# Kernel optimization log

Measured on AMD Instinct MI355X. Metric: run time of the kernel, lower is better.

Reference implementation:

```python
import jax, jax.numpy as jnp
import numpy as np

BLOCK = 16
WINDOW = 6
NSEG = BLOCK - WINDOW + 1  # 11
ACT_TH = 0.1
IMP_TH = 0.1


def _gauss_kernel(size=7, sigma=7.0 / 6):
    m = (size - 1) / 2.0
    y, x = np.mgrid[-m:m + 1, -m:m + 1]
    h = np.exp(-(x * x + y * y) / (2.0 * sigma * sigma))
    h[h < np.finfo(h.dtype).eps * h.max()] = 0
    h /= h.sum()
    return jnp.asarray(h, dtype=jnp.float32)


def _normalize_with_gauss(img):
    # MSCN normalization: (img - mu) / (std + 1), gaussian 7x7 sigma=7/6, replicate pad
    k = _gauss_kernel()[None, None]  # [1,1,7,7]
    pad = 3
    p = jnp.pad(img, ((0, 0), (0, 0), (pad, pad), (pad, pad)), mode='edge')
    conv = lambda z: jax.lax.conv_general_dilated(z, k, (1, 1), 'VALID')
    mu = conv(p)
    mu2 = conv(p * p)
    std = jnp.sqrt(jnp.abs(mu2 - mu * mu))
    return (img - mu) / (std + 1.0)


def _seg_std_min(edge):
    # edge: [..., 16]; sliding windows of length 6 at offsets 0..10 (matches segment_edge)
    segs = jnp.stack([edge[..., i:i + WINDOW] for i in range(NSEG)], axis=-2)  # [...,11,6]
    return jnp.min(jnp.std(segs, axis=-1, ddof=1), axis=-1)


def _piqe_core(x):
    B, C, H, W = x.shape
    img = jnp.round(255.0 * x / jnp.max(x.reshape(B, -1), axis=-1)[:, None, None, None])
    col_pad, row_pad = W % BLOCK, H % BLOCK
    img = jnp.pad(img, ((0, 0), (0, 0), (0, row_pad), (0, col_pad)), mode='symmetric')
    n = _normalize_with_gauss(img)

    nbh, nbw = H // BLOCK, W // BLOCK
    blk = n[:, 0].reshape(B, nbh, BLOCK, nbw, BLOCK).transpose(0, 1, 3, 2, 4)  # [B,nbh,nbw,16,16]

    block_var = jnp.var(blk, axis=(-2, -1), ddof=1)  # unbiased
    active = block_var > ACT_TH

    # noticeable distortion: any edge sliding-segment std below threshold
    edges = (blk[..., 0, :], blk[..., :, BLOCK - 1], blk[..., BLOCK - 1, :], blk[..., :, 0])
    impaired = jnp.zeros_like(active)
    for e in edges:
        impaired = impaired | (_seg_std_min(e) < IMP_TH)

    # noise criterion: center-surround deviation (faithful to original indexing:
    # center = columns 7,8; surround excludes columns 7 and 9)
    center = jnp.concatenate([blk[..., :, 7], blk[..., :, 8]], axis=-1)  # [...,32]
    sur_cols = jnp.array([0, 1, 2, 3, 4, 5, 6, 8, 10, 11, 12, 13, 14, 15])
    sur = blk[..., :, sur_cols].reshape(B, nbh, nbw, -1)  # [...,224]
    csd = jnp.std(center, axis=-1, ddof=1) / jnp.std(sur, axis=-1, ddof=1)
    csd = jnp.where(jnp.isnan(csd), 0.0, csd)
    sigma = jnp.sqrt(block_var)
    beta = jnp.abs(sigma - csd) / jnp.maximum(sigma, csd)
    wnc = sigma > 2.0 * beta

    contrib = active * (impaired * (1.0 - block_var) + wnc * block_var)
    nhsa = jnp.sum(active, axis=(1, 2))
    score = (jnp.sum(contrib, axis=(1, 2)) + 1.0) / (1.0 + nhsa) * 100.0

    def expand(mb):  # [B,nbh,nbw] bool -> [B,1,H,W]
        return jnp.repeat(jnp.repeat(mb, BLOCK, axis=1), BLOCK, axis=2)[:, None]

    na_mask = expand(active & impaired)[..., :H, :W]
    noise_mask = expand(active & wnc)[..., :H, :W]
    act_mask = expand(active)[..., :H, :W]
    return score, na_mask, noise_mask, act_mask


def setup_inputs() -> dict:
    key = jax.random.key(0)
    x = jax.random.uniform(key, (8, 1, 2048, 2048), dtype=jnp.float32)
    return {"x": x}


def reference(x):
    score, na_mask, noise_mask, act_mask = _piqe_core(x)
    return score  # PIQE.forward returns results[0]
```

## Files before the change

### kernel.cpp

```cpp
#include <hip/hip_runtime.h>
#include <math.h>

#define IH 2048
#define IW 2048
#define NBATCH 8
#define TILE 64
#define HALO 3
#define SIW 70
#define SI 71
#define ACT_TH 0.1f
#define IMP_TH 0.1f

#define TGRID 2048
#define NTILES 8192

#define G0 0.0125602013f
#define G1 0.0788279697f
#define G2 0.2372960895f
#define G3 0.3426314790f

__device__ __forceinline__ float fsqrt_f(float x) { return __builtin_amdgcn_sqrtf(x); }
__device__ __forceinline__ float frcp_f(float x)  { return __builtin_amdgcn_rcpf(x); }

__device__ __forceinline__ void piqe_tile(
    const float* __restrict__ img0, float scale,
    float* __restrict__ contrib_sum, unsigned int* __restrict__ nhsa,
    int b, int ox, int oy, int tid)
{
    __shared__ float s_img[SIW * SI];
    __shared__ float s_c;
    __shared__ unsigned int s_a;

    if (tid == 0) { s_c = 0.0f; s_a = 0u; }

    if (ox != 0 && oy != 0 && ox != IW - TILE && oy != IH - TILE) {
        const float* base = img0 + (size_t)(oy - HALO) * IW + (ox - HALO);
        for (int i = tid; i < SIW * SIW; i += 256) {
            int r = i / SIW, c = i - r * SIW;
            s_img[r * SI + c] = rintf(base[r * IW + c] * scale);
        }
    } else {
        for (int i = tid; i < SIW * SIW; i += 256) {
            int r = i / SIW, c = i - r * SIW;
            int gy = oy + r - HALO; gy = max(0, min(IH - 1, gy));
            int gx = ox + c - HALO; gx = max(0, min(IW - 1, gx));
            s_img[r * SI + c] = rintf(img0[(size_t)gy * IW + gx] * scale);
        }
    }
    __syncthreads();

    const float gk[7] = {G0, G1, G2, G3, G2, G1, G0};
    const int cc = tid & 63;
    const int gg = tid >> 6;
    const int r0 = gg * 16;
    const float* bp = &s_img[r0 * SI + cc];

    float hm[7], h2[7], pv[4], nv[16];
#pragma unroll
    for (int j = 0; j < 22; ++j) {
        float m = 0.0f, m2 = 0.0f, ctr = 0.0f;
#pragma unroll
        for (int k = 0; k < 7; ++k) {
            float v = bp[j * SI + k];
            if (k == 3) ctr = v;
            m = fmaf(gk[k], v, m);
            m2 = fmaf(gk[k] * v, v, m2);
        }
        hm[j % 7] = m;
        h2[j % 7] = m2;
        if (j >= 3 && j <= 18) pv[(j - 3) & 3] = ctr;
        if (j >= 6) {
            const int r = j - 6;
            float vm = 0.0f, vm2 = 0.0f;
#pragma unroll
            for (int k = 0; k < 7; ++k) {
                vm = fmaf(gk[k], hm[(r + k) % 7], vm);
                vm2 = fmaf(gk[k], h2[(r + k) % 7], vm2);
            }
            float sd = fsqrt_f(fabsf(vm2 - vm * vm));
            nv[r] = (pv[r & 3] - vm) * frcp_f(sd + 1.0f);
        }
    }
    __syncthreads();

    {
        float* wp = &s_img[(r0 + HALO) * SI + (cc + HALO)];
#pragma unroll
        for (int r = 0; r < 16; ++r) wp[r * SI] = nv[r];
    }
    __syncthreads();

    const int lane = tid & 63;
    const int wv = tid >> 6;
    const int blk = wv * 4 + (lane >> 4);
    const int L = lane & 15;
    const int bi = blk >> 2, bj = blk & 3;
    const float* np0 = &s_img[(HALO + bi * 16) * SI + (HALO + bj * 16)];

    float rv[16];
    float s1 = 0.0f, s2 = 0.0f;
#pragma unroll
    for (int k = 0; k < 16; ++k) {
        float v = np0[L * SI + k];
        rv[k] = v;
        s1 += v;
        s2 += v * v;
    }
    float c1 = rv[7] + rv[8];
    float c2 = rv[7] * rv[7] + rv[8] * rv[8];
    float u1 = s1 - rv[7] - rv[9];
    float u2 = s2 - rv[7] * rv[7] - rv[9] * rv[9];

    float minstd = __builtin_inff();
    if (L < 4) {
        int offs, stp;
        if (L == 0)      { offs = 0;       stp = 1; }
        else if (L == 1) { offs = 15 * SI; stp = 1; }
        else if (L == 2) { offs = 0;       stp = SI; }
        else             { offs = 15;      stp = SI; }
        float e[16];
#pragma unroll
        for (int k = 0; k < 16; ++k) e[k] = np0[offs + k * stp];
        float w1 = 0.0f, w2 = 0.0f;
#pragma unroll
        for (int k = 0; k < 6; ++k) { w1 += e[k]; w2 += e[k] * e[k]; }
#pragma unroll
        for (int i = 0; i < 11; ++i) {
            float var = (w2 - w1 * w1 * (1.0f / 6.0f)) * (1.0f / 5.0f);
            minstd = fminf(minstd, fsqrt_f(fmaxf(var, 0.0f)));
            if (i < 10) {
                w1 += e[i + 6] - e[i];
                w2 += e[i + 6] * e[i + 6] - e[i] * e[i];
            }
        }
    }

#pragma unroll
    for (int m = 1; m < 16; m <<= 1) {
        s1 += __shfl_xor(s1, m);
        s2 += __shfl_xor(s2, m);
        c1 += __shfl_xor(c1, m);
        c2 += __shfl_xor(c2, m);
        u1 += __shfl_xor(u1, m);
        u2 += __shfl_xor(u2, m);
        minstd = fminf(minstd, __shfl_xor(minstd, m));
    }

    if (L == 0) {
        float bv = fmaxf((s2 - s1 * s1 * (1.0f / 256.0f)) * (1.0f / 255.0f), 0.0f);
        bool active = bv > ACT_TH;
        float cstd = fsqrt_f(fmaxf((c2 - c1 * c1 * (1.0f / 32.0f)) * (1.0f / 31.0f), 0.0f));
        float sstd = fsqrt_f(fmaxf((u2 - u1 * u1 * (1.0f / 224.0f)) * (1.0f / 223.0f), 0.0f));
        float csd = cstd * frcp_f(sstd);
        if (csd != csd) csd = 0.0f;
        float sigma = fsqrt_f(bv);
        float beta = fabsf(sigma - csd) * frcp_f(fmaxf(sigma, csd));
        bool wnc = sigma > 2.0f * beta;
        bool impaired = minstd < IMP_TH;
        if (active) {
            float contrib = (impaired ? (1.0f - bv) : 0.0f) + (wnc ? bv : 0.0f);
            atomicAdd(&s_c, contrib);
            atomicAdd(&s_a, 1u);
        }
    }
    __syncthreads();
    if (tid == 0) {
        atomicAdd(&contrib_sum[b], s_c);
        atomicAdd(&nhsa[b], s_a);
    }
}

__global__ __launch_bounds__(256) void batch_max_kernel(
    const float* __restrict__ x, unsigned int* __restrict__ maxbits)
{
    const int b = blockIdx.y;
    const float4* p = (const float4*)(x + (size_t)b * (size_t)(IH * IW));
    const int n4 = IH * IW / 4;
    float m = 0.0f;
    for (int i = blockIdx.x * blockDim.x + threadIdx.x; i < n4;
         i += gridDim.x * blockDim.x) {
        float4 v = p[i];
        m = fmaxf(m, fmaxf(fmaxf(v.x, v.y), fmaxf(v.z, v.w)));
    }
#pragma unroll
    for (int s = 1; s < 64; s <<= 1) m = fmaxf(m, __shfl_xor(m, s));
    __shared__ float sm[4];
    const int lane = threadIdx.x & 63, wv = threadIdx.x >> 6;
    if (lane == 0) sm[wv] = m;
    __syncthreads();
    if (threadIdx.x == 0) {
        m = fmaxf(fmaxf(sm[0], sm[1]), fmaxf(sm[2], sm[3]));
        atomicMax(&maxbits[b], __float_as_uint(m));
    }
}

__global__ __launch_bounds__(256) void piqe_tiles_kernel(
    const float* __restrict__ x, const unsigned int* __restrict__ maxbits,
    float* __restrict__ contrib_sum, unsigned int* __restrict__ nhsa,
    unsigned int* __restrict__ ticket, float* __restrict__ out)
{
    const int tid = threadIdx.x;

#pragma unroll 1
    for (int t = blockIdx.x; t < NTILES; t += TGRID) {
        const int b = t >> 10;
        const int tt = t & 1023;
        const int oy = (tt >> 5) * TILE;
        const int ox = (tt & 31) * TILE;
        const float* img0 = x + (size_t)b * (size_t)(IH * IW);
        const float scale = 255.0f / __uint_as_float(maxbits[b]);
        piqe_tile(img0, scale, contrib_sum, nhsa, b, ox, oy, tid);
    }

    __shared__ unsigned int s_win;
    if (tid == 0) {
        unsigned int tk = __hip_atomic_fetch_add(
            ticket, 1u, __ATOMIC_ACQ_REL, __HIP_MEMORY_SCOPE_AGENT);
        s_win = (tk == (unsigned int)(TGRID - 1)) ? 1u : 0u;
    }
    __syncthreads();
    if (s_win && tid < NBATCH) {
        float c = __hip_atomic_load(&contrib_sum[tid], __ATOMIC_RELAXED,
                                    __HIP_MEMORY_SCOPE_AGENT);
        unsigned int a = __hip_atomic_load(&nhsa[tid], __ATOMIC_RELAXED,
                                           __HIP_MEMORY_SCOPE_AGENT);
        out[tid] = (c + 1.0f) / (1.0f + (float)a) * 100.0f;
    }
}

extern "C" void kernel_launch(void* const* d_in, const int* in_sizes, int n_in,
                              void* d_out, int out_size, void* d_ws, size_t ws_size,
                              hipStream_t stream)
{
    const float* x = (const float*)d_in[0];
    float* out = (float*)d_out;

    unsigned int* maxbits = (unsigned int*)d_ws;
    float* contrib = (float*)((char*)d_ws + 32);
    unsigned int* nhsa = (unsigned int*)((char*)d_ws + 64);
    unsigned int* ticket = (unsigned int*)((char*)d_ws + 96);

    hipMemsetAsync(d_ws, 0, 128, stream);
    batch_max_kernel<<<dim3(256, NBATCH), 256, 0, stream>>>(x, maxbits);
    piqe_tiles_kernel<<<dim3(TGRID), 256, 0, stream>>>(
        x, maxbits, contrib, nhsa, ticket, out);
}
```

Before: 368.8 us.

## Launch one block per tile with row-wise halo loads and unrolled max reduction

Replaces the grid-stride loop over 8192 tiles (2048 persistent blocks) with a 3D grid of one block per 64x64 tile, and updates the completion ticket to count all tiles. Tile staging now has each wavefront load whole rows, removing per-element div/mod and giving coalesced row reads. The batch-max kernel uses a fixed unrolled trip count instead of a runtime stride loop. More blocks mean more launch and scheduling overhead and more global atomics on the ticket and partial sums, traded for simpler indexing and better load balance.

```diff
diff --git a/kernel.cpp b/kernel.cpp
--- a/kernel.cpp
+++ b/kernel.cpp
@@ -10,8 +10,6 @@
 #define SI 71
 #define ACT_TH 0.1f
 #define IMP_TH 0.1f
-
-#define TGRID 2048
 #define NTILES 8192
 
 #define G0 0.0125602013f
@@ -22,29 +20,72 @@
 __device__ __forceinline__ float fsqrt_f(float x) { return __builtin_amdgcn_sqrtf(x); }
 __device__ __forceinline__ float frcp_f(float x)  { return __builtin_amdgcn_rcpf(x); }
 
-__device__ __forceinline__ void piqe_tile(
-    const float* __restrict__ img0, float scale,
+#define MAXBLK 256
+#define MAXSTride (MAXBLK * 256)
+__global__ __launch_bounds__(256) void batch_max_kernel(
+    const float* __restrict__ x, unsigned int* __restrict__ maxbits)
+{
+    const int b = blockIdx.y;
+    const float4* p = (const float4*)(x + (size_t)b * (size_t)(IH * IW));
+    float m = 0.0f;
+    int i = blockIdx.x * 256 + threadIdx.x;
+#pragma unroll
+    for (int it = 0; it < (IH * IW / 4) / MAXSTride; ++it, i += MAXSTride) {
+        float4 v = p[i];
+        m = fmaxf(m, fmaxf(fmaxf(v.x, v.y), fmaxf(v.z, v.w)));
+    }
+#pragma unroll
+    for (int s = 1; s < 64; s <<= 1) m = fmaxf(m, __shfl_xor(m, s));
+    __shared__ float sm[4];
+    const int lane = threadIdx.x & 63, wv = threadIdx.x >> 6;
+    if (lane == 0) sm[wv] = m;
+    __syncthreads();
+    if (threadIdx.x == 0) {
+        m = fmaxf(fmaxf(sm[0], sm[1]), fmaxf(sm[2], sm[3]));
+        atomicMax(&maxbits[b], __float_as_uint(m));
+    }
+}
+
+__global__ __launch_bounds__(256) void piqe_main_kernel(
+    const float* __restrict__ x, const unsigned int* __restrict__ maxbits,
     float* __restrict__ contrib_sum, unsigned int* __restrict__ nhsa,
-    int b, int ox, int oy, int tid)
+    unsigned int* __restrict__ ticket, float* __restrict__ out)
 {
     __shared__ float s_img[SIW * SI];
     __shared__ float s_c;
     __shared__ unsigned int s_a;
 
+    const int tid = threadIdx.x;
+    const int b = blockIdx.z;
+    const int ox = blockIdx.x * TILE;
+    const int oy = blockIdx.y * TILE;
+    const float* img0 = x + (size_t)b * (size_t)(IH * IW);
+    const float scale = 255.0f / __uint_as_float(maxbits[b]);
+
     if (tid == 0) { s_c = 0.0f; s_a = 0u; }
 
-    if (ox != 0 && oy != 0 && ox != IW - TILE && oy != IH - TILE) {
-        const float* base = img0 + (size_t)(oy - HALO) * IW + (ox - HALO);
-        for (int i = tid; i < SIW * SIW; i += 256) {
-            int r = i / SIW, c = i - r * SIW;
-            s_img[r * SI + c] = rintf(base[r * IW + c] * scale);
-        }
-    } else {
-        for (int i = tid; i < SIW * SIW; i += 256) {
-            int r = i / SIW, c = i - r * SIW;
-            int gy = oy + r - HALO; gy = max(0, min(IH - 1, gy));
-            int gx = ox + c - HALO; gx = max(0, min(IW - 1, gx));
-            s_img[r * SI + c] = rintf(img0[(size_t)gy * IW + gx] * scale);
+    {
+        const int lane = tid & 63, wvv = tid >> 6;
+        if (ox != 0 && oy != 0 && ox != IW - TILE && oy != IH - TILE) {
+            const float* base = img0 + (size_t)(oy - HALO) * IW + (ox - HALO);
+            for (int r = wvv; r < SIW; r += 4) {
+                const float* rowp = base + (size_t)r * IW;
+                float* srow = &s_img[r * SI];
+                srow[lane] = rintf(rowp[lane] * scale);
+                if (lane < 6) srow[64 + lane] = rintf(rowp[64 + lane] * scale);
+            }
+        } else {
+            for (int r = wvv; r < SIW; r += 4) {
+                int gy = oy + r - HALO; gy = max(0, min(IH - 1, gy));
+                const float* rowp = img0 + (size_t)gy * IW;
+                float* srow = &s_img[r * SI];
+                int gx = ox + lane - HALO; gx = max(0, min(IW - 1, gx));
+                srow[lane] = rintf(rowp[gx] * scale);
+                if (lane < 6) {
+                    int gx2 = ox + 64 + lane - HALO; gx2 = max(0, min(IW - 1, gx2));
+                    srow[64 + lane] = rintf(rowp[gx2] * scale);
+                }
+            }
         }
     }
     __syncthreads();
@@ -168,55 +209,12 @@
         atomicAdd(&contrib_sum[b], s_c);
         atomicAdd(&nhsa[b], s_a);
     }
-}
-
-__global__ __launch_bounds__(256) void batch_max_kernel(
-    const float* __restrict__ x, unsigned int* __restrict__ maxbits)
-{
-    const int b = blockIdx.y;
-    const float4* p = (const float4*)(x + (size_t)b * (size_t)(IH * IW));
-    const int n4 = IH * IW / 4;
-    float m = 0.0f;
-    for (int i = blockIdx.x * blockDim.x + threadIdx.x; i < n4;
-         i += gridDim.x * blockDim.x) {
-        float4 v = p[i];
-        m = fmaxf(m, fmaxf(fmaxf(v.x, v.y), fmaxf(v.z, v.w)));
-    }
-#pragma unroll
-    for (int s = 1; s < 64; s <<= 1) m = fmaxf(m, __shfl_xor(m, s));
-    __shared__ float sm[4];
-    const int lane = threadIdx.x & 63, wv = threadIdx.x >> 6;
-    if (lane == 0) sm[wv] = m;
-    __syncthreads();
-    if (threadIdx.x == 0) {
-        m = fmaxf(fmaxf(sm[0], sm[1]), fmaxf(sm[2], sm[3]));
-        atomicMax(&maxbits[b], __float_as_uint(m));
-    }
-}
-
-__global__ __launch_bounds__(256) void piqe_tiles_kernel(
-    const float* __restrict__ x, const unsigned int* __restrict__ maxbits,
-    float* __restrict__ contrib_sum, unsigned int* __restrict__ nhsa,
-    unsigned int* __restrict__ ticket, float* __restrict__ out)
-{
-    const int tid = threadIdx.x;
-
-#pragma unroll 1
-    for (int t = blockIdx.x; t < NTILES; t += TGRID) {
-        const int b = t >> 10;
-        const int tt = t & 1023;
-        const int oy = (tt >> 5) * TILE;
-        const int ox = (tt & 31) * TILE;
-        const float* img0 = x + (size_t)b * (size_t)(IH * IW);
-        const float scale = 255.0f / __uint_as_float(maxbits[b]);
-        piqe_tile(img0, scale, contrib_sum, nhsa, b, ox, oy, tid);
-    }
 
     __shared__ unsigned int s_win;
     if (tid == 0) {
         unsigned int tk = __hip_atomic_fetch_add(
             ticket, 1u, __ATOMIC_ACQ_REL, __HIP_MEMORY_SCOPE_AGENT);
-        s_win = (tk == (unsigned int)(TGRID - 1)) ? 1u : 0u;
+        s_win = (tk == (unsigned int)(NTILES - 1)) ? 1u : 0u;
     }
     __syncthreads();
     if (s_win && tid < NBATCH) {
@@ -241,7 +239,7 @@
     unsigned int* ticket = (unsigned int*)((char*)d_ws + 96);
 
     hipMemsetAsync(d_ws, 0, 128, stream);
-    batch_max_kernel<<<dim3(256, NBATCH), 256, 0, stream>>>(x, maxbits);
-    piqe_tiles_kernel<<<dim3(TGRID), 256, 0, stream>>>(
+    batch_max_kernel<<<dim3(MAXBLK, NBATCH), 256, 0, stream>>>(x, maxbits);
+    piqe_main_kernel<<<dim3(IW / TILE, IH / TILE, NBATCH), 256, 0, stream>>>(
         x, maxbits, contrib, nhsa, ticket, out);
 }
```

Result: slower. 448.6 us (+21.6%).
